# Kernel optimization log

Hardware: AMD Instinct MI355X
Metric: run time of the kernel (lower is better)

## Reference

```python
import jax, jax.numpy as jnp
import numpy as np

NQ = 4          # n_qubits
NL = 2          # ansatz layers in timestep circuit
T = 200         # n_timesteps
DEG = 3         # qsvt_degree
B = 2048        # batch
NROTS = 5 * NQ * NL     # 40
QFF_NROTS = 5 * NQ      # 20
DIM = 2 ** NQ

# --- batched 2x2 gate matrices (h = theta/2, shape (N,)) ---
def _rx(h):
    c = jnp.cos(h).astype(jnp.complex64)
    s = (-1j * jnp.sin(h)).astype(jnp.complex64)
    return jnp.stack([jnp.stack([c, s], -1), jnp.stack([s, c], -1)], -2)

def _ry(h):
    c, s = jnp.cos(h), jnp.sin(h)
    return jnp.stack([jnp.stack([c, -s], -1), jnp.stack([s, c], -1)], -2).astype(jnp.complex64)

def _rz(h):
    e = jnp.exp(-1j * h.astype(jnp.complex64))
    z = jnp.zeros_like(e)
    return jnp.stack([jnp.stack([e, z], -1), jnp.stack([z, jnp.conj(e)], -1)], -2)

# state layout: (N, 2, 2, ..., 2) with axis 1+w = qubit w (PennyLane wire ordering)
def _apply_1q(state, mat, w):
    st = jnp.moveaxis(state, 1 + w, -1)
    st = jnp.einsum('bij,b...j->b...i', mat, st)
    return jnp.moveaxis(st, -1, 1 + w)

def _apply_crx(state, h, cw, tw):
    m = _rx(h)
    st = jnp.moveaxis(state, (1 + cw, 1 + tw), (-2, -1))  # (..., control, target)
    s1 = jnp.einsum('bij,b...j->b...i', m, st[..., 1, :])  # RX on target iff control=1
    st = jnp.stack([st[..., 0, :], s1], axis=-2)
    return jnp.moveaxis(st, (-2, -1), (1 + cw, 1 + tw))

def _ansatz(state, params, layers):
    # params: (N, 5*NQ*layers) float
    half = params * 0.5
    idx = 0
    for _ in range(layers):
        for i in range(NQ):
            state = _apply_1q(state, _rx(half[:, idx]), i)
            state = _apply_1q(state, _ry(half[:, idx + 1]), i)
            state = _apply_1q(state, _rz(half[:, idx + 2]), i)
            idx += 3
        for i in range(NQ):
            state = _apply_crx(state, half[:, idx], i, (i + 1) % NQ)
            idx += 1
        for i in range(NQ - 1, -1, -1):
            state = _apply_crx(state, half[:, idx], i, (i - 1) % NQ)
            idx += 1
    return state

def _lcu(base, tparams, coeffs):
    # base: (B, DIM) complex; tparams: (B, T, NROTS); coeffs: (B, T) complex
    b, t, r = tparams.shape
    flat = tparams.reshape(b * t, r)
    st = jnp.repeat(base, t, axis=0).reshape((b * t,) + (2,) * NQ)
    st = _ansatz(st, flat, NL)
    ev = st.reshape(b, t, DIM)
    return jnp.einsum('bti,bt->bi', ev, coeffs)

def _expvals(state):
    # returns (B, 3*NQ): [<X_0..X_{n-1}>, <Y...>, <Z...>]
    outs_x, outs_y, outs_z = [], [], []
    red = tuple(range(1, NQ))  # reduce all non-batch, non-target axes after moveaxis
    for i in range(NQ):
        st = jnp.moveaxis(state, 1 + i, -1)
        s0, s1 = st[..., 0], st[..., 1]
        z = jnp.conj(s0) * s1
        outs_x.append(jnp.sum(2.0 * jnp.real(z), axis=red))
        outs_y.append(jnp.sum(2.0 * jnp.imag(z), axis=red))
        outs_z.append(jnp.sum(jnp.abs(s0) ** 2 - jnp.abs(s1) ** 2, axis=red))
    return jnp.stack(outs_x + outs_y + outs_z, axis=1).astype(jnp.float32)

def _forward(timestep_params, poly_coeffs, mix_re, mix_im, qff_params):
    b = timestep_params.shape[0]
    base = jnp.zeros((b, DIM), jnp.complex64).at[:, 0].set(1.0)
    coeffs = jnp.broadcast_to((mix_re + 1j * mix_im).astype(jnp.complex64), (b, T))
    # QSVT polynomial: acc = sum_k c_k (LCU)^k |0>
    acc = poly_coeffs[0] * base
    work = base
    for k in range(1, DEG + 1):
        work = _lcu(work, timestep_params, coeffs)
        acc = acc + poly_coeffs[k] * work
    acc = acc / jnp.sum(jnp.abs(poly_coeffs))  # L1 norm of poly coeffs
    norm = jnp.linalg.norm(acc, axis=1, keepdims=True)
    st = (acc / (norm + 1e-9)).reshape((b,) + (2,) * NQ)
    qp = jnp.broadcast_to(qff_params, (b, QFF_NROTS))
    st = _ansatz(st, qp, 1)
    return _expvals(st)

def setup_inputs() -> dict:
    key = jax.random.key(0)
    k1, k2, k3, k4, k5 = jax.random.split(key, 5)
    return {
        'timestep_params': jax.random.uniform(k1, (B, T, NROTS), jnp.float32),
        'poly_coeffs': jax.random.uniform(k2, (DEG + 1,), jnp.float32),
        'mix_re': jax.random.uniform(k3, (T,), jnp.float32),
        'mix_im': jax.random.uniform(k4, (T,), jnp.float32),
        'qff_params': jax.random.uniform(k5, (QFF_NROTS,), jnp.float32),
    }

def reference(timestep_params, poly_coeffs, mix_re, mix_im, qff_params):
    return _forward(timestep_params, poly_coeffs, mix_re, mix_im, qff_params)
```

## Files before the change

### kernel.cpp

```cpp
#include <hip/hip_runtime.h>
#include <math.h>

#define TSTEPS 200
#define NROTS  40
#define BLK    256
#define DEG    3

#define FMAF __builtin_fmaf

__device__ __forceinline__ void fsc(float h, float& s, float& c) {
    s = __sinf(h); c = __cosf(h);
}

__device__ __forceinline__ void make_u(float h1, float h2, float h3, float* u) {
    float s1, c1, s2, c2, s3, c3;
    fsc(h1, s1, c1); fsc(h2, s2, c2); fsc(h3, s3, c3);
    float A = c1 * c2, Bv = s1 * s2, C = c1 * s2, D = s1 * c2;
    u[0] = FMAF( s3, Bv, c3 * A);
    u[1] = FMAF(-s3, A,  c3 * Bv);
    u[2] = -FMAF(s3, D,  c3 * C);
    u[3] = FMAF(-c3, D,  s3 * C);
}

template<int BIT>
__device__ __forceinline__ void g_u2(float* V, const float* u) {
    const float u00r = u[0], u00i = u[1], u01r = u[2], u01i = u[3];
    #pragma unroll
    for (int p = 0; p < 16; ++p) {
        if (p & BIT) continue;
        const int q = p | BIT;
        float a0r = V[p], a0i = V[16 + p], a1r = V[q], a1i = V[16 + q];
        float t0 = u00r * a0r;
        t0 = FMAF(-u00i, a0i, t0);
        t0 = FMAF( u01r, a1r, t0);
        t0 = FMAF(-u01i, a1i, t0);
        float t1 = u00r * a0i;
        t1 = FMAF( u00i, a0r, t1);
        t1 = FMAF( u01r, a1i, t1);
        t1 = FMAF( u01i, a1r, t1);
        float t2 = u00r * a1r;
        t2 = FMAF( u00i, a1i, t2);
        t2 = FMAF(-u01r, a0r, t2);
        t2 = FMAF(-u01i, a0i, t2);
        float t3 = u00r * a1i;
        t3 = FMAF(-u00i, a1r, t3);
        t3 = FMAF(-u01r, a0i, t3);
        t3 = FMAF( u01i, a0r, t3);
        V[p] = t0; V[16 + p] = t1; V[q] = t2; V[16 + q] = t3;
    }
}

template<int CBIT, int TBIT>
__device__ __forceinline__ void g_crx_pre(float* V, float s, float c) {
    #pragma unroll
    for (int p = 0; p < 16; ++p) {
        if (!(p & CBIT) || (p & TBIT)) continue;
        const int q = p | TBIT;
        float a0r = V[p], a0i = V[16 + p], a1r = V[q], a1i = V[16 + q];
        V[p]      = FMAF( s, a1i, c * a0r);
        V[16 + p] = FMAF(-s, a1r, c * a0i);
        V[q]      = FMAF( s, a0i, c * a1r);
        V[16 + q] = FMAF(-s, a0r, c * a1i);
    }
}

__device__ __forceinline__ void apply_layer_pre(float* V, const float (&u)[4][4],
                                                const float (&cs)[8][2]) {
    g_u2<8>(V, u[0]); g_u2<4>(V, u[1]); g_u2<2>(V, u[2]); g_u2<1>(V, u[3]);
    g_crx_pre<8, 4>(V, cs[0][0], cs[0][1]);
    g_crx_pre<4, 2>(V, cs[1][0], cs[1][1]);
    g_crx_pre<2, 1>(V, cs[2][0], cs[2][1]);
    g_crx_pre<1, 8>(V, cs[3][0], cs[3][1]);
    g_crx_pre<1, 2>(V, cs[4][0], cs[4][1]);
    g_crx_pre<2, 4>(V, cs[5][0], cs[5][1]);
    g_crx_pre<4, 8>(V, cs[6][0], cs[6][1]);
    g_crx_pre<8, 1>(V, cs[7][0], cs[7][1]);
}

template<int S, int HALF>
__device__ __forceinline__ void rstep(float* V, int lane) {
    const bool hi = (lane >> S) & 1;
    #pragma unroll
    for (int j = 0; j < HALF; ++j) {
        float send = hi ? V[j] : V[j + HALF];
        float keep = hi ? V[j + HALF] : V[j];
        V[j] = keep + __shfl_xor(send, 1 << S, 64);
    }
}

extern "C" __global__ void __launch_bounds__(BLK)
qac_kernel(const float* __restrict__ tp,
           const float* __restrict__ poly,
           const float* __restrict__ mixr,
           const float* __restrict__ mixi,
           const float* __restrict__ qff,
           float* __restrict__ out)
{
    __shared__ float s_red[4][32];
    __shared__ float s_w[32];
    __shared__ float s_acc[32];

    const int b    = blockIdx.x;
    const int tid  = threadIdx.x;
    const int lane = tid & 63;
    const int wv   = tid >> 6;

    if (tid < 32) {
        s_w[tid]   = (tid == 0) ? 1.f : 0.f;
        s_acc[tid] = (tid == 0) ? poly[0] : 0.f;
    }

    float cr_ = 0.f, ci_ = 0.f;
    if (tid < TSTEPS) { cr_ = mixr[tid]; ci_ = mixi[tid]; }
    const int mt = (tid < TSTEPS) ? tid : (TSTEPS - 1);
    const float4* p4 = (const float4*)(tp + (size_t)b * (TSTEPS * NROTS) + mt * NROTS);

    float tu[2][4][4];
    float tc[2][8][2];
    #pragma unroll
    for (int L = 0; L < 2; ++L) {
        float4 f0 = p4[5*L+0], f1 = p4[5*L+1], f2v = p4[5*L+2], f3 = p4[5*L+3], f4 = p4[5*L+4];
        make_u(0.5f*f0.x,  0.5f*f0.y,  0.5f*f0.z,  tu[L][0]);
        make_u(0.5f*f0.w,  0.5f*f1.x,  0.5f*f1.y,  tu[L][1]);
        make_u(0.5f*f1.z,  0.5f*f1.w,  0.5f*f2v.x, tu[L][2]);
        make_u(0.5f*f2v.y, 0.5f*f2v.z, 0.5f*f2v.w, tu[L][3]);
        fsc(0.5f*f3.x, tc[L][0][0], tc[L][0][1]);
        fsc(0.5f*f3.y, tc[L][1][0], tc[L][1][1]);
        fsc(0.5f*f3.z, tc[L][2][0], tc[L][2][1]);
        fsc(0.5f*f3.w, tc[L][3][0], tc[L][3][1]);
        fsc(0.5f*f4.x, tc[L][4][0], tc[L][4][1]);
        fsc(0.5f*f4.y, tc[L][5][0], tc[L][5][1]);
        fsc(0.5f*f4.z, tc[L][6][0], tc[L][6][1]);
        fsc(0.5f*f4.w, tc[L][7][0], tc[L][7][1]);
    }

    const int vidx = ((lane & 1) << 4) | ((lane & 2) << 2) | (lane & 4) |
                     ((lane & 8) >> 2) | ((lane & 16) >> 4);

    __syncthreads();

    #pragma unroll 1
    for (int k = 1; k <= DEG; ++k) {
        float V[32];
        {
            const float4* s4 = (const float4*)s_w;
            #pragma unroll
            for (int i = 0; i < 8; ++i) {
                float4 f = s4[i];
                V[4*i + 0] = f.x; V[4*i + 1] = f.y;
                V[4*i + 2] = f.z; V[4*i + 3] = f.w;
            }
        }

        apply_layer_pre(V, tu[0], tc[0]);
        apply_layer_pre(V, tu[1], tc[1]);

        #pragma unroll
        for (int i = 0; i < 16; ++i) {
            float r = V[i], im = V[16 + i];
            V[i]      = FMAF(-im, ci_, r * cr_);
            V[16 + i] = FMAF( im, cr_, r * ci_);
        }

        rstep<0, 16>(V, lane);
        rstep<1, 8>(V, lane);
        rstep<2, 4>(V, lane);
        rstep<3, 2>(V, lane);
        rstep<4, 1>(V, lane);
        float tot = V[0] + __shfl_xor(V[0], 32, 64);
        if (lane < 32) s_red[wv][vidx] = tot;

        __syncthreads();
        if (tid < 32) {
            float r = s_red[0][tid] + s_red[1][tid] + s_red[2][tid] + s_red[3][tid];
            s_w[tid] = r;
            s_acc[tid] += poly[k] * r;
        }
        __syncthreads();
    }

    if (tid < 16) {
        const int l = tid;
        float l1 = fabsf(poly[0]) + fabsf(poly[1]) + fabsf(poly[2]) + fabsf(poly[3]);
        float inv = 1.f / l1;
        float ar = s_acc[l] * inv, ai = s_acc[16 + l] * inv;
        float n2 = ar * ar + ai * ai;
        #pragma unroll
        for (int o = 1; o < 16; o <<= 1) n2 += __shfl_xor(n2, o, 64);
        float sc = 1.f / (sqrtf(n2) + 1e-9f);
        ar *= sc; ai *= sc;

        float s, c, pr, pi, se, ce, t0;
        #pragma unroll
        for (int w = 0; w < 4; ++w) {
            const int BIT = 8 >> w;
            fsc(0.5f * qff[3 * w + 0], s, c);
            pr = __shfl_xor(ar, BIT, 64); pi = __shfl_xor(ai, BIT, 64);
            t0 = c * ar + s * pi; ai = c * ai - s * pr; ar = t0;
            fsc(0.5f * qff[3 * w + 1], s, c);
            pr = __shfl_xor(ar, BIT, 64); pi = __shfl_xor(ai, BIT, 64);
            se = (l & BIT) ? s : -s;
            t0 = c * ar + se * pr; ai = c * ai + se * pi; ar = t0;
            fsc(0.5f * qff[3 * w + 2], s, c);
            se = (l & BIT) ? s : -s;
            t0 = c * ar - se * ai; ai = c * ai + se * ar; ar = t0;
        }
        #define CRXF(CB, TB, hp) { fsc(0.5f * (hp), s, c);                        \
            pr = __shfl_xor(ar, TB, 64); pi = __shfl_xor(ai, TB, 64);             \
            ce = (l & CB) ? c : 1.f; se = (l & CB) ? s : 0.f;                     \
            t0 = ce * ar + se * pi; ai = ce * ai - se * pr; ar = t0; }
        CRXF(8, 4, qff[12]) CRXF(4, 2, qff[13]) CRXF(2, 1, qff[14]) CRXF(1, 8, qff[15])
        CRXF(1, 2, qff[16]) CRXF(2, 4, qff[17]) CRXF(4, 8, qff[18]) CRXF(8, 1, qff[19])
        #undef CRXF

        float* o = out + (size_t)b * 12;
        #pragma unroll
        for (int w = 0; w < 4; ++w) {
            const int BIT = 8 >> w;
            pr = __shfl_xor(ar, BIT, 64); pi = __shfl_xor(ai, BIT, 64);
            float m = (l & BIT) ? 0.f : 1.f;
            float X = m * 2.f * (ar * pr + ai * pi);
            float Y = m * 2.f * (ar * pi - ai * pr);
            float Z = m * (ar * ar + ai * ai - pr * pr - pi * pi);
            #pragma unroll
            for (int of = 1; of < 16; of <<= 1) {
                X += __shfl_xor(X, of, 64);
                Y += __shfl_xor(Y, of, 64);
                Z += __shfl_xor(Z, of, 64);
            }
            if (l == 0) { o[w] = X; o[4 + w] = Y; o[8 + w] = Z; }
        }
    }
}

extern "C" void kernel_launch(void* const* d_in, const int* in_sizes, int n_in,
                              void* d_out, int out_size, void* d_ws, size_t ws_size,
                              hipStream_t stream) {
    const float* tp   = (const float*)d_in[0];
    const float* poly = (const float*)d_in[1];
    const float* mixr = (const float*)d_in[2];
    const float* mixi = (const float*)d_in[3];
    const float* qff  = (const float*)d_in[4];
    float* out = (float*)d_out;
    const int B = in_sizes[0] / (TSTEPS * NROTS);
    qac_kernel<<<dim3(B), dim3(BLK), 0, stream>>>(tp, poly, mixr, mixi, qff, out);
}
```

Baseline: 145.9 us.

## Use one wavefront per batch element, looping timesteps in register-accumulated slots

Shrinks the block from four waves to a single 64-lane wave per batch element. Each lane now walks four timestep slots and accumulates the mixed, rotated states in registers, so the shared-memory cross-wave reduction buffer goes away. The cost is that the timestep parameters are reloaded and the trig and gate matrices recomputed in every QSVT degree iteration, instead of being computed once and kept in registers. This trades lower synchronisation and LDS traffic for roughly three times the transcendental work and serial per-wave latency.

```diff
diff --git a/kernel.cpp b/kernel.cpp
--- a/kernel.cpp
+++ b/kernel.cpp
@@ -3,8 +3,9 @@
 
 #define TSTEPS 200
 #define NROTS  40
-#define BLK    256
+#define BLK    64
 #define DEG    3
+#define NSLOT  4
 
 #define FMAF __builtin_fmaf
 
@@ -88,7 +89,7 @@
     }
 }
 
-extern "C" __global__ void __launch_bounds__(BLK)
+extern "C" __global__ void __launch_bounds__(BLK, 2)
 qac_kernel(const float* __restrict__ tp,
            const float* __restrict__ poly,
            const float* __restrict__ mixr,
@@ -96,43 +97,18 @@
            const float* __restrict__ qff,
            float* __restrict__ out)
 {
-    __shared__ float s_red[4][32];
-    __shared__ float s_w[32];
+    __shared__ __align__(16) float s_w[32];
     __shared__ float s_acc[32];
 
     const int b    = blockIdx.x;
-    const int tid  = threadIdx.x;
-    const int lane = tid & 63;
-    const int wv   = tid >> 6;
-
-    if (tid < 32) {
-        s_w[tid]   = (tid == 0) ? 1.f : 0.f;
-        s_acc[tid] = (tid == 0) ? poly[0] : 0.f;
-    }
-
-    float cr_ = 0.f, ci_ = 0.f;
-    if (tid < TSTEPS) { cr_ = mixr[tid]; ci_ = mixi[tid]; }
-    const int mt = (tid < TSTEPS) ? tid : (TSTEPS - 1);
-    const float4* p4 = (const float4*)(tp + (size_t)b * (TSTEPS * NROTS) + mt * NROTS);
-
-    float tu[2][4][4];
-    float tc[2][8][2];
-    #pragma unroll
-    for (int L = 0; L < 2; ++L) {
-        float4 f0 = p4[5*L+0], f1 = p4[5*L+1], f2v = p4[5*L+2], f3 = p4[5*L+3], f4 = p4[5*L+4];
-        make_u(0.5f*f0.x,  0.5f*f0.y,  0.5f*f0.z,  tu[L][0]);
-        make_u(0.5f*f0.w,  0.5f*f1.x,  0.5f*f1.y,  tu[L][1]);
-        make_u(0.5f*f1.z,  0.5f*f1.w,  0.5f*f2v.x, tu[L][2]);
-        make_u(0.5f*f2v.y, 0.5f*f2v.z, 0.5f*f2v.w, tu[L][3]);
-        fsc(0.5f*f3.x, tc[L][0][0], tc[L][0][1]);
-        fsc(0.5f*f3.y, tc[L][1][0], tc[L][1][1]);
-        fsc(0.5f*f3.z, tc[L][2][0], tc[L][2][1]);
-        fsc(0.5f*f3.w, tc[L][3][0], tc[L][3][1]);
-        fsc(0.5f*f4.x, tc[L][4][0], tc[L][4][1]);
-        fsc(0.5f*f4.y, tc[L][5][0], tc[L][5][1]);
-        fsc(0.5f*f4.z, tc[L][6][0], tc[L][6][1]);
-        fsc(0.5f*f4.w, tc[L][7][0], tc[L][7][1]);
-    }
+    const int lane = threadIdx.x;
+
+    if (lane < 32) {
+        s_w[lane]   = (lane == 0) ? 1.f : 0.f;
+        s_acc[lane] = (lane == 0) ? poly[0] : 0.f;
+    }
+
+    const float* base = tp + (size_t)b * (TSTEPS * NROTS);
 
     const int vidx = ((lane & 1) << 4) | ((lane & 2) << 2) | (lane & 4) |
                      ((lane & 8) >> 2) | ((lane & 16) >> 4);
@@ -141,46 +117,80 @@
 
     #pragma unroll 1
     for (int k = 1; k <= DEG; ++k) {
-        float V[32];
-        {
-            const float4* s4 = (const float4*)s_w;
+        asm volatile("" : "+v"(base));
+
+        const float pk = poly[k];
+        float P[32];
+        #pragma unroll
+        for (int i = 0; i < 32; ++i) P[i] = 0.f;
+
+        #pragma unroll 1
+        for (int s = 0; s < NSLOT; ++s) {
+            const int t = lane + 64 * s;
+            const bool valid = (t < TSTEPS);
+            const int mt = valid ? t : (TSTEPS - 1);
+            const float cr_ = valid ? mixr[t] : 0.f;
+            const float ci_ = valid ? mixi[t] : 0.f;
+            const float4* p4 = (const float4*)(base + mt * NROTS);
+
+            float tu[2][4][4];
+            float tc[2][8][2];
             #pragma unroll
-            for (int i = 0; i < 8; ++i) {
-                float4 f = s4[i];
-                V[4*i + 0] = f.x; V[4*i + 1] = f.y;
-                V[4*i + 2] = f.z; V[4*i + 3] = f.w;
-            }
-        }
-
-        apply_layer_pre(V, tu[0], tc[0]);
-        apply_layer_pre(V, tu[1], tc[1]);
-
-        #pragma unroll
-        for (int i = 0; i < 16; ++i) {
-            float r = V[i], im = V[16 + i];
-            V[i]      = FMAF(-im, ci_, r * cr_);
-            V[16 + i] = FMAF( im, cr_, r * ci_);
-        }
-
-        rstep<0, 16>(V, lane);
-        rstep<1, 8>(V, lane);
-        rstep<2, 4>(V, lane);
-        rstep<3, 2>(V, lane);
-        rstep<4, 1>(V, lane);
-        float tot = V[0] + __shfl_xor(V[0], 32, 64);
-        if (lane < 32) s_red[wv][vidx] = tot;
+            for (int L = 0; L < 2; ++L) {
+                float4 f0 = p4[5*L+0], f1 = p4[5*L+1], f2v = p4[5*L+2],
+                       f3 = p4[5*L+3], f4 = p4[5*L+4];
+                make_u(0.5f*f0.x,  0.5f*f0.y,  0.5f*f0.z,  tu[L][0]);
+                make_u(0.5f*f0.w,  0.5f*f1.x,  0.5f*f1.y,  tu[L][1]);
+                make_u(0.5f*f1.z,  0.5f*f1.w,  0.5f*f2v.x, tu[L][2]);
+                make_u(0.5f*f2v.y, 0.5f*f2v.z, 0.5f*f2v.w, tu[L][3]);
+                fsc(0.5f*f3.x, tc[L][0][0], tc[L][0][1]);
+                fsc(0.5f*f3.y, tc[L][1][0], tc[L][1][1]);
+                fsc(0.5f*f3.z, tc[L][2][0], tc[L][2][1]);
+                fsc(0.5f*f3.w, tc[L][3][0], tc[L][3][1]);
+                fsc(0.5f*f4.x, tc[L][4][0], tc[L][4][1]);
+                fsc(0.5f*f4.y, tc[L][5][0], tc[L][5][1]);
+                fsc(0.5f*f4.z, tc[L][6][0], tc[L][6][1]);
+                fsc(0.5f*f4.w, tc[L][7][0], tc[L][7][1]);
+            }
+
+            float V[32];
+            {
+                const float4* s4 = (const float4*)s_w;
+                #pragma unroll
+                for (int i = 0; i < 8; ++i) {
+                    float4 f = s4[i];
+                    V[4*i + 0] = f.x; V[4*i + 1] = f.y;
+                    V[4*i + 2] = f.z; V[4*i + 3] = f.w;
+                }
+            }
+            apply_layer_pre(V, tu[0], tc[0]);
+            apply_layer_pre(V, tu[1], tc[1]);
+
+            #pragma unroll
+            for (int i = 0; i < 16; ++i) {
+                float r = V[i], im = V[16 + i];
+                P[i]      = FMAF(r, cr_, FMAF(-im, ci_, P[i]));
+                P[16 + i] = FMAF(r, ci_, FMAF( im, cr_, P[16 + i]));
+            }
+        }
+
+        rstep<0, 16>(P, lane);
+        rstep<1, 8>(P, lane);
+        rstep<2, 4>(P, lane);
+        rstep<3, 2>(P, lane);
+        rstep<4, 1>(P, lane);
+        float tot = P[0] + __shfl_xor(P[0], 32, 64);
 
         __syncthreads();
-        if (tid < 32) {
-            float r = s_red[0][tid] + s_red[1][tid] + s_red[2][tid] + s_red[3][tid];
-            s_w[tid] = r;
-            s_acc[tid] += poly[k] * r;
+        if (lane < 32) {
+            s_w[vidx]   = tot;
+            s_acc[vidx] = FMAF(pk, tot, s_acc[vidx]);
         }
         __syncthreads();
     }
 
-    if (tid < 16) {
-        const int l = tid;
+    if (lane < 16) {
+        const int l = lane;
         float l1 = fabsf(poly[0]) + fabsf(poly[1]) + fabsf(poly[2]) + fabsf(poly[3]);
         float inv = 1.f / l1;
         float ar = s_acc[l] * inv, ai = s_acc[16 + l] * inv;
```

New measurement: 172.3 us. 18.1% more time.
